# Kernel optimization log

Measured on AMD Instinct MI355X. Metric: run time of the kernel, lower is better.

## Reference

```python
import jax, jax.numpy as jnp
import numpy as np

IN_C = 256
KEY_C = 256
VAL_C = 256
HEADS = 8


def setup_inputs() -> dict:
    key = jax.random.key(0)
    ks = jax.random.split(key, 9)
    s = 0.02
    return {
        "x": jax.random.normal(ks[0], (4, 8192, IN_C), dtype=jnp.float32),
        "Wk": jax.random.normal(ks[1], (KEY_C, IN_C), dtype=jnp.float32) * s,
        "bk": jax.random.normal(ks[2], (KEY_C,), dtype=jnp.float32) * s,
        "Wq": jax.random.normal(ks[3], (KEY_C, IN_C), dtype=jnp.float32) * s,
        "bq": jax.random.normal(ks[4], (KEY_C,), dtype=jnp.float32) * s,
        "Wv": jax.random.normal(ks[5], (VAL_C, IN_C), dtype=jnp.float32) * s,
        "bv": jax.random.normal(ks[6], (VAL_C,), dtype=jnp.float32) * s,
        "Wr": jax.random.normal(ks[7], (IN_C, VAL_C), dtype=jnp.float32) * s,
        "br": jax.random.normal(ks[8], (IN_C,), dtype=jnp.float32) * s,
    }


def reference(x, Wk, bk, Wq, bq, Wv, bv, Wr, br):
    n, N, c = x.shape
    # Faithful to torch: reshape (NOT transpose) of (n, N, c) into (n, c, N)
    xi = x.reshape(n, c, N)
    # 1x1 convs == channel-mixing matmuls over the token axis
    K = jnp.einsum('oc,ncs->nos', Wk, xi) + bk[None, :, None]
    Q = jnp.einsum('oc,ncs->nos', Wq, xi) + bq[None, :, None]
    V = jnp.einsum('oc,ncs->nos', Wv, xi) + bv[None, :, None]
    dk = KEY_C // HEADS
    dv = VAL_C // HEADS
    Kh = K.reshape(n, HEADS, dk, N)
    Qh = Q.reshape(n, HEADS, dk, N)
    Vh = V.reshape(n, HEADS, dv, N)
    # keys: softmax over tokens (dim=2); queries: softmax over head key channels (dim=1)
    Kh = jax.nn.softmax(Kh, axis=3)
    Qh = jax.nn.softmax(Qh, axis=2)
    # context = K @ V^T : [n, H, dk, dv]
    ctx = jnp.einsum('nhks,nhvs->nhkv', Kh, Vh)
    # attended = context^T @ Q : [n, H, dv, N]
    att = jnp.einsum('nhkv,nhks->nhvs', ctx, Qh)
    agg = att.reshape(n, VAL_C, N)
    rep = jnp.einsum('ov,nvs->nos', Wr, agg) + br[None, :, None]
    out = rep + xi  # residual in (n, c, N) layout
    return jnp.transpose(out, (0, 2, 1))  # (n, N, c)
```

## Files before the change

### kernel.cpp

```cpp
#include <hip/hip_runtime.h>

#define NTOK 8192
#define NCH  256
#define TT   64
#define XTP  264
#define EKP  72

typedef unsigned short u16;
typedef __attribute__((ext_vector_type(8))) short bf16x8;
typedef __attribute__((ext_vector_type(4))) float f32x4;
typedef __attribute__((ext_vector_type(8))) unsigned short u16x8;
typedef __attribute__((ext_vector_type(4))) unsigned short u16x4;

__device__ __forceinline__ float b2f(u16 h){
  union{unsigned u; float f;} x; x.u = ((unsigned)h) << 16; return x.f;
}
__device__ __forceinline__ u16 f2b(float f){
  union{float f; unsigned u;} x; x.f = f;
  unsigned u = x.u;
  return (u16)((u + 0x7FFFu + ((u >> 16) & 1u)) >> 16);
}
__device__ __forceinline__ f32x4 mfma16(bf16x8 a, bf16x8 b, f32x4 c){
  return __builtin_amdgcn_mfma_f32_16x16x32_bf16(a, b, c, 0, 0, 0);
}

__device__ __forceinline__ void stage_xtile(const float* __restrict__ xb,
                                            u16* scratch, u16* dst, int t)
{
  #pragma unroll
  for (int i = 0; i < 4; ++i) {
    int ch = i * 64 + (t >> 3);
    int tk = (t & 7) * 8;
    const float* p = xb + (size_t)ch * NTOK + tk;
    float4 v0 = *(const float4*)p;
    float4 v1 = *(const float4*)(p + 4);
    u16x8 pk;
    pk[0]=f2b(v0.x); pk[1]=f2b(v0.y); pk[2]=f2b(v0.z); pk[3]=f2b(v0.w);
    pk[4]=f2b(v1.x); pk[5]=f2b(v1.y); pk[6]=f2b(v1.z); pk[7]=f2b(v1.w);
    *(u16x8*)&scratch[ch * EKP + tk] = pk;
  }
  __syncthreads();
  #pragma unroll
  for (int p = 0; p < 4; ++p) {
    int idx = p * 512 + t;
    int tok = idx & 63;
    int ch = (idx >> 6) * 8;
    u16x8 o;
    #pragma unroll
    for (int j = 0; j < 8; ++j) o[j] = scratch[(ch + j) * EKP + tok];
    *(u16x8*)&dst[tok * XTP + ch] = o;
  }
}

__global__ __launch_bounds__(256)
void k_prep(const float* __restrict__ Wk, const float* __restrict__ Wq,
            const float* __restrict__ Wv, const float* __restrict__ Wr,
            u16* __restrict__ wbf, float* __restrict__ ctxAcc)
{
  const int t = threadIdx.x, bid = blockIdx.x;
  if (bid < 64) {
    const int mat = bid >> 4;
    const float* src = (mat == 0) ? Wk : (mat == 1) ? Wq : (mat == 2) ? Wv : Wr;
    u16* dst = wbf + mat * 65536;
    const int base = (bid & 15) * 4096 + t * 16;
    #pragma unroll
    for (int i = 0; i < 4; ++i) {
      float4 v = *(const float4*)(src + base + i * 4);
      u16x4 pk; pk[0]=f2b(v.x); pk[1]=f2b(v.y); pk[2]=f2b(v.z); pk[3]=f2b(v.w);
      *(u16x4*)(dst + base + i * 4) = pk;
    }
  } else {
    int j = (bid - 64) * 1024 + t * 4;
    float4 z; z.x = z.y = z.z = z.w = 0.f;
    *(float4*)(ctxAcc + j) = z;
  }
}

__global__ __launch_bounds__(512, 4)
void k_ctx(const float* __restrict__ x, const u16* __restrict__ wbf,
           const float* __restrict__ bk, const float* __restrict__ bv,
           float* __restrict__ ctxAcc, float* __restrict__ denomAcc)
{
  __shared__ u16 bufA[NCH * EKP];
  __shared__ u16 ekb[NCH * EKP];

  const int t = threadIdx.x;
  const int b = blockIdx.x >> 7, g = blockIdx.x & 127;
  const int w = t >> 6, lane = t & 63;
  const int l15 = lane & 15, quad = lane >> 4;
  const u16* Wkb = wbf;
  const u16* Wvb = wbf + 2 * 65536;

  stage_xtile(x + (size_t)b * NCH * NTOK + g * TT, ekb, bufA, t);
  __syncthreads();

  f32x4 acc[2][4];

  #pragma unroll
  for (int mi = 0; mi < 2; ++mi)
    #pragma unroll
    for (int nj = 0; nj < 4; ++nj) acc[mi][nj] = (f32x4)0.f;
  for (int k0 = 0; k0 < NCH; k0 += 32) {
    bf16x8 af[2], bx[4];
    #pragma unroll
    for (int mi = 0; mi < 2; ++mi)
      af[mi] = *(const bf16x8*)(Wkb + (size_t)(w * 32 + mi * 16 + l15) * NCH + k0 + quad * 8);
    #pragma unroll
    for (int nj = 0; nj < 4; ++nj)
      bx[nj] = *(const bf16x8*)&bufA[(nj * 16 + l15) * XTP + k0 + quad * 8];
    #pragma unroll
    for (int mi = 0; mi < 2; ++mi)
      #pragma unroll
      for (int nj = 0; nj < 4; ++nj) acc[mi][nj] = mfma16(af[mi], bx[nj], acc[mi][nj]);
  }
  #pragma unroll
  for (int mi = 0; mi < 2; ++mi) {
    float4 bb = *(const float4*)(bk + w * 32 + mi * 16 + quad * 4);
    #pragma unroll
    for (int nj = 0; nj < 4; ++nj) {
      int tok = nj * 16 + l15, chb = w * 32 + mi * 16 + quad * 4;
      ekb[(chb + 0) * EKP + tok] = f2b(__expf(acc[mi][nj][0] + bb.x));
      ekb[(chb + 1) * EKP + tok] = f2b(__expf(acc[mi][nj][1] + bb.y));
      ekb[(chb + 2) * EKP + tok] = f2b(__expf(acc[mi][nj][2] + bb.z));
      ekb[(chb + 3) * EKP + tok] = f2b(__expf(acc[mi][nj][3] + bb.w));
    }
  }

  #pragma unroll
  for (int mi = 0; mi < 2; ++mi)
    #pragma unroll
    for (int nj = 0; nj < 4; ++nj) acc[mi][nj] = (f32x4)0.f;
  for (int k0 = 0; k0 < NCH; k0 += 32) {
    bf16x8 af[2], bx[4];
    #pragma unroll
    for (int mi = 0; mi < 2; ++mi)
      af[mi] = *(const bf16x8*)(Wvb + (size_t)(w * 32 + mi * 16 + l15) * NCH + k0 + quad * 8);
    #pragma unroll
    for (int nj = 0; nj < 4; ++nj)
      bx[nj] = *(const bf16x8*)&bufA[(nj * 16 + l15) * XTP + k0 + quad * 8];
    #pragma unroll
    for (int mi = 0; mi < 2; ++mi)
      #pragma unroll
      for (int nj = 0; nj < 4; ++nj) acc[mi][nj] = mfma16(af[mi], bx[nj], acc[mi][nj]);
  }
  __syncthreads();
  #pragma unroll
  for (int mi = 0; mi < 2; ++mi) {
    float4 bb = *(const float4*)(bv + w * 32 + mi * 16 + quad * 4);
    #pragma unroll
    for (int nj = 0; nj < 4; ++nj) {
      int tok = nj * 16 + l15, chb = w * 32 + mi * 16 + quad * 4;
      bufA[(chb + 0) * EKP + tok] = f2b(acc[mi][nj][0] + bb.x);
      bufA[(chb + 1) * EKP + tok] = f2b(acc[mi][nj][1] + bb.y);
      bufA[(chb + 2) * EKP + tok] = f2b(acc[mi][nj][2] + bb.z);
      bufA[(chb + 3) * EKP + tok] = f2b(acc[mi][nj][3] + bb.w);
    }
  }
  __syncthreads();

  f32x4 cacc[2][2];
  #pragma unroll
  for (int mi = 0; mi < 2; ++mi)
    #pragma unroll
    for (int nj = 0; nj < 2; ++nj) cacc[mi][nj] = (f32x4)0.f;
  #pragma unroll
  for (int kc = 0; kc < 2; ++kc) {
    bf16x8 ae[2], bvv[2];
    #pragma unroll
    for (int mi = 0; mi < 2; ++mi)
      ae[mi] = *(const bf16x8*)&ekb[(w * 32 + mi * 16 + l15) * EKP + kc * 32 + quad * 8];
    #pragma unroll
    for (int nj = 0; nj < 2; ++nj)
      bvv[nj] = *(const bf16x8*)&bufA[(w * 32 + nj * 16 + l15) * EKP + kc * 32 + quad * 8];
    #pragma unroll
    for (int mi = 0; mi < 2; ++mi)
      #pragma unroll
      for (int nj = 0; nj < 2; ++nj)
        cacc[mi][nj] = mfma16(ae[mi], bvv[nj], cacc[mi][nj]);
  }
  float dsum = 0.f;
  if (t < 256) {
    #pragma unroll
    for (int s = 0; s < TT; s += 8) {
      u16x8 v = *(const u16x8*)&ekb[t * EKP + s];
      #pragma unroll
      for (int j = 0; j < 8; ++j) dsum += b2f(v[j]);
    }
  }

  float* cp = ctxAcc + ((size_t)b << 13);
  #pragma unroll
  for (int mi = 0; mi < 2; ++mi)
    #pragma unroll
    for (int nj = 0; nj < 2; ++nj)
      #pragma unroll
      for (int r = 0; r < 4; ++r) {
        int e = ((w * 32 + mi * 16 + quad * 4 + r) << 5) + nj * 16 + l15;
        atomicAdd(&cp[e], cacc[mi][nj][r]);
      }
  if (t < 256)
    atomicAdd(&denomAcc[b * 256 + t], dsum);
}

__global__ __launch_bounds__(512, 4)
void k_out(const float* __restrict__ x, const u16* __restrict__ wbf,
           const float* __restrict__ bq, const float* __restrict__ br,
           const float* __restrict__ ctxAcc, const float* __restrict__ denomAcc,
           float* __restrict__ out)
{
  __shared__ u16 xs[TT * XTP];
  __shared__ u16 qs[NCH * EKP];

  const int t = threadIdx.x;
  const int b = blockIdx.x >> 7, g = blockIdx.x & 127;
  const int w = t >> 6, lane = t & 63;
  const int l15 = lane & 15, quad = lane >> 4;
  const u16* Wqb = wbf + 65536;
  const u16* Wrb = wbf + 3 * 65536;

  stage_xtile(x + (size_t)b * NCH * NTOK + g * TT, qs, xs, t);
  __syncthreads();

  const float* cb = ctxAcc + ((size_t)b << 13) + ((size_t)w << 10);
  bf16x8 ac[2];
  #pragma unroll
  for (int mi = 0; mi < 2; ++mi)
    #pragma unroll
    for (int j = 0; j < 8; ++j)
      ac[mi][j] = (short)f2b(cb[(quad * 8 + j) * 32 + mi * 16 + l15]);

  f32x4 acc[2][4];
  #pragma unroll
  for (int mi = 0; mi < 2; ++mi)
    #pragma unroll
    for (int nj = 0; nj < 4; ++nj) acc[mi][nj] = (f32x4)0.f;
  for (int k0 = 0; k0 < NCH; k0 += 32) {
    bf16x8 af[2], bx[4];
    #pragma unroll
    for (int mi = 0; mi < 2; ++mi)
      af[mi] = *(const bf16x8*)(Wqb + (size_t)(w * 32 + mi * 16 + l15) * NCH + k0 + quad * 8);
    #pragma unroll
    for (int nj = 0; nj < 4; ++nj)
      bx[nj] = *(const bf16x8*)&xs[(nj * 16 + l15) * XTP + k0 + quad * 8];
    #pragma unroll
    for (int mi = 0; mi < 2; ++mi)
      #pragma unroll
      for (int nj = 0; nj < 4; ++nj) acc[mi][nj] = mfma16(af[mi], bx[nj], acc[mi][nj]);
  }
  #pragma unroll
  for (int mi = 0; mi < 2; ++mi) {
    float4 bb = *(const float4*)(bq + w * 32 + mi * 16 + quad * 4);
    #pragma unroll
    for (int nj = 0; nj < 4; ++nj) {
      acc[mi][nj][0] = __expf(acc[mi][nj][0] + bb.x);
      acc[mi][nj][1] = __expf(acc[mi][nj][1] + bb.y);
      acc[mi][nj][2] = __expf(acc[mi][nj][2] + bb.z);
      acc[mi][nj][3] = __expf(acc[mi][nj][3] + bb.w);
    }
  }
  float inv[4];
  #pragma unroll
  for (int nj = 0; nj < 4; ++nj) {
    float s = 0.f;
    #pragma unroll
    for (int mi = 0; mi < 2; ++mi)
      #pragma unroll
      for (int r = 0; r < 4; ++r) s += acc[mi][nj][r];
    s += __shfl_xor(s, 16);
    s += __shfl_xor(s, 32);
    inv[nj] = 1.0f / s;
  }
  #pragma unroll
  for (int mi = 0; mi < 2; ++mi) {
    float4 dv = *(const float4*)(denomAcc + b * 256 + w * 32 + mi * 16 + quad * 4);
    float rdx = 1.0f / dv.x, rdy = 1.0f / dv.y, rdz = 1.0f / dv.z, rdw = 1.0f / dv.w;
    #pragma unroll
    for (int nj = 0; nj < 4; ++nj) {
      u16x4 pk;
      pk[0] = f2b(acc[mi][nj][0] * inv[nj] * rdx);
      pk[1] = f2b(acc[mi][nj][1] * inv[nj] * rdy);
      pk[2] = f2b(acc[mi][nj][2] * inv[nj] * rdz);
      pk[3] = f2b(acc[mi][nj][3] * inv[nj] * rdw);
      *(u16x4*)&qs[(nj * 16 + l15) * XTP + w * 32 + mi * 16 + quad * 4] = pk;
    }
  }
  __syncthreads();

  f32x4 aacc[2][4];
  {
    #pragma unroll
    for (int nj = 0; nj < 4; ++nj) {
      bf16x8 bqf = *(const bf16x8*)&qs[(nj * 16 + l15) * XTP + w * 32 + quad * 8];
      #pragma unroll
      for (int mi = 0; mi < 2; ++mi)
        aacc[mi][nj] = mfma16(ac[mi], bqf, (f32x4)0.f);
    }
  }
  #pragma unroll
  for (int mi = 0; mi < 2; ++mi)
    #pragma unroll
    for (int nj = 0; nj < 4; ++nj) {
      u16x4 pk;
      pk[0] = f2b(aacc[mi][nj][0]);
      pk[1] = f2b(aacc[mi][nj][1]);
      pk[2] = f2b(aacc[mi][nj][2]);
      pk[3] = f2b(aacc[mi][nj][3]);
      *(u16x4*)&qs[(nj * 16 + l15) * XTP + w * 32 + mi * 16 + quad * 4] = pk;
    }
  __syncthreads();

  #pragma unroll
  for (int mi = 0; mi < 2; ++mi)
    #pragma unroll
    for (int nj = 0; nj < 4; ++nj) acc[mi][nj] = (f32x4)0.f;
  for (int k0 = 0; k0 < NCH; k0 += 32) {
    bf16x8 af[2], bx[4];
    #pragma unroll
    for (int mi = 0; mi < 2; ++mi)
      af[mi] = *(const bf16x8*)(Wrb + (size_t)(w * 32 + mi * 16 + l15) * NCH + k0 + quad * 8);
    #pragma unroll
    for (int nj = 0; nj < 4; ++nj)
      bx[nj] = *(const bf16x8*)&qs[(nj * 16 + l15) * XTP + k0 + quad * 8];
    #pragma unroll
    for (int mi = 0; mi < 2; ++mi)
      #pragma unroll
      for (int nj = 0; nj < 4; ++nj) acc[mi][nj] = mfma16(af[mi], bx[nj], acc[mi][nj]);
  }
  #pragma unroll
  for (int mi = 0; mi < 2; ++mi) {
    float4 bb = *(const float4*)(br + w * 32 + mi * 16 + quad * 4);
    #pragma unroll
    for (int nj = 0; nj < 4; ++nj) {
      int tok = nj * 16 + l15;
      u16x4 rx = *(const u16x4*)&xs[tok * XTP + w * 32 + mi * 16 + quad * 4];
      float4 o;
      o.x = acc[mi][nj][0] + bb.x + b2f(rx[0]);
      o.y = acc[mi][nj][1] + bb.y + b2f(rx[1]);
      o.z = acc[mi][nj][2] + bb.z + b2f(rx[2]);
      o.w = acc[mi][nj][3] + bb.w + b2f(rx[3]);
      *(float4*)(out + (((size_t)(b * NTOK + g * TT + tok)) << 8) + w * 32 + mi * 16 + quad * 4) = o;
    }
  }
}

extern "C" void kernel_launch(void* const* d_in, const int* in_sizes, int n_in,
                              void* d_out, int out_size, void* d_ws, size_t ws_size,
                              hipStream_t stream) {
  const float* x  = (const float*)d_in[0];
  const float* Wk = (const float*)d_in[1];
  const float* bk = (const float*)d_in[2];
  const float* Wq = (const float*)d_in[3];
  const float* bq = (const float*)d_in[4];
  const float* Wv = (const float*)d_in[5];
  const float* bv = (const float*)d_in[6];
  const float* Wr = (const float*)d_in[7];
  const float* br = (const float*)d_in[8];
  float* out = (float*)d_out;

  char* wsb = (char*)d_ws;
  float* ctxAcc   = (float*)wsb;
  float* denomAcc = (float*)(wsb + 131072);
  u16*   wbf      = (u16*)(wsb + 135168);

  hipLaunchKernelGGL(k_prep, dim3(97), dim3(256), 0, stream,
                     Wk, Wq, Wv, Wr, wbf, ctxAcc);
  hipLaunchKernelGGL(k_ctx, dim3(512), dim3(512), 0, stream,
                     x, wbf, bk, bv, ctxAcc, denomAcc);
  hipLaunchKernelGGL(k_out, dim3(512), dim3(512), 0, stream,
                     x, wbf, bq, br, ctxAcc, denomAcc, out);
}
```

Measured before the change: 150.9 us.

## Replace global atomics with per-block partials and a separate reduction kernel

k_ctx now writes each block's context partial (as bf16) and its denominator partial to workspace instead of issuing float atomicAdds into a shared accumulator. A new k_red kernel sums the 128 partials per batch, stores the context transposed in bf16 so k_out can load it with one vector load, and precomputes reciprocal denominators. This removes atomic contention and the zero-init pass, at the cost of an extra launch, about 8 MB of partial traffic, and bf16 rounding of the partials before summation.

Result: faster. 144.9 us (-4.0%).

```diff
diff --git a/kernel.cpp b/kernel.cpp
--- a/kernel.cpp
+++ b/kernel.cpp
@@ -55,31 +55,25 @@
 __global__ __launch_bounds__(256)
 void k_prep(const float* __restrict__ Wk, const float* __restrict__ Wq,
             const float* __restrict__ Wv, const float* __restrict__ Wr,
-            u16* __restrict__ wbf, float* __restrict__ ctxAcc)
+            u16* __restrict__ wbf)
 {
   const int t = threadIdx.x, bid = blockIdx.x;
-  if (bid < 64) {
-    const int mat = bid >> 4;
-    const float* src = (mat == 0) ? Wk : (mat == 1) ? Wq : (mat == 2) ? Wv : Wr;
-    u16* dst = wbf + mat * 65536;
-    const int base = (bid & 15) * 4096 + t * 16;
-    #pragma unroll
-    for (int i = 0; i < 4; ++i) {
-      float4 v = *(const float4*)(src + base + i * 4);
-      u16x4 pk; pk[0]=f2b(v.x); pk[1]=f2b(v.y); pk[2]=f2b(v.z); pk[3]=f2b(v.w);
-      *(u16x4*)(dst + base + i * 4) = pk;
-    }
-  } else {
-    int j = (bid - 64) * 1024 + t * 4;
-    float4 z; z.x = z.y = z.z = z.w = 0.f;
-    *(float4*)(ctxAcc + j) = z;
+  const int mat = bid >> 4;
+  const float* src = (mat == 0) ? Wk : (mat == 1) ? Wq : (mat == 2) ? Wv : Wr;
+  u16* dst = wbf + mat * 65536;
+  const int base = (bid & 15) * 4096 + t * 16;
+  #pragma unroll
+  for (int i = 0; i < 4; ++i) {
+    float4 v = *(const float4*)(src + base + i * 4);
+    u16x4 pk; pk[0]=f2b(v.x); pk[1]=f2b(v.y); pk[2]=f2b(v.z); pk[3]=f2b(v.w);
+    *(u16x4*)(dst + base + i * 4) = pk;
   }
 }
 
 __global__ __launch_bounds__(512, 4)
 void k_ctx(const float* __restrict__ x, const u16* __restrict__ wbf,
            const float* __restrict__ bk, const float* __restrict__ bv,
-           float* __restrict__ ctxAcc, float* __restrict__ denomAcc)
+           u16* __restrict__ ctxPart, float* __restrict__ denomPart)
 {
   __shared__ u16 bufA[NCH * EKP];
   __shared__ u16 ekb[NCH * EKP];
@@ -188,7 +182,7 @@
     }
   }
 
-  float* cp = ctxAcc + ((size_t)b << 13);
+  u16* cp = ctxPart + ((size_t)(b * 128 + g) << 13);
   #pragma unroll
   for (int mi = 0; mi < 2; ++mi)
     #pragma unroll
@@ -196,16 +190,45 @@
       #pragma unroll
       for (int r = 0; r < 4; ++r) {
         int e = ((w * 32 + mi * 16 + quad * 4 + r) << 5) + nj * 16 + l15;
-        atomicAdd(&cp[e], cacc[mi][nj][r]);
+        cp[e] = f2b(cacc[mi][nj][r]);
       }
   if (t < 256)
-    atomicAdd(&denomAcc[b * 256 + t], dsum);
+    denomPart[(size_t)(b * 128 + g) * 256 + t] = dsum;
+}
+
+__global__ __launch_bounds__(256)
+void k_red(const u16* __restrict__ ctxPart, const float* __restrict__ denomPart,
+           u16* __restrict__ ctxT, float* __restrict__ rdenomF)
+{
+  int i = blockIdx.x * 256 + threadIdx.x;
+  if (i < 32768) {
+    int b = i >> 13, e = i & 8191;
+    const u16* p = ctxPart + ((size_t)(b * 128) << 13) + e;
+    float s0 = 0.f, s1 = 0.f, s2 = 0.f, s3 = 0.f;
+    #pragma unroll 8
+    for (int g = 0; g < 128; g += 4) {
+      s0 += b2f(p[(size_t)(g + 0) << 13]);
+      s1 += b2f(p[(size_t)(g + 1) << 13]);
+      s2 += b2f(p[(size_t)(g + 2) << 13]);
+      s3 += b2f(p[(size_t)(g + 3) << 13]);
+    }
+    float s = (s0 + s1) + (s2 + s3);
+    int hh = e >> 10, kk = (e >> 5) & 31, vch = e & 31;
+    ctxT[(((b * 8 + hh) * 32 + vch) << 5) + kk] = f2b(s);
+  } else if (i < 33792) {
+    int j = i - 32768, b = j >> 8, ch = j & 255;
+    const float* p = denomPart + (size_t)(b * 128) * 256 + ch;
+    float s = 0.f;
+    #pragma unroll 8
+    for (int g = 0; g < 128; ++g) s += p[(size_t)g << 8];
+    rdenomF[j] = 1.0f / s;
+  }
 }
 
 __global__ __launch_bounds__(512, 4)
 void k_out(const float* __restrict__ x, const u16* __restrict__ wbf,
            const float* __restrict__ bq, const float* __restrict__ br,
-           const float* __restrict__ ctxAcc, const float* __restrict__ denomAcc,
+           const u16* __restrict__ ctxT, const float* __restrict__ rdenomF,
            float* __restrict__ out)
 {
   __shared__ u16 xs[TT * XTP];
@@ -221,13 +244,10 @@
   stage_xtile(x + (size_t)b * NCH * NTOK + g * TT, qs, xs, t);
   __syncthreads();
 
-  const float* cb = ctxAcc + ((size_t)b << 13) + ((size_t)w << 10);
   bf16x8 ac[2];
   #pragma unroll
   for (int mi = 0; mi < 2; ++mi)
-    #pragma unroll
-    for (int j = 0; j < 8; ++j)
-      ac[mi][j] = (short)f2b(cb[(quad * 8 + j) * 32 + mi * 16 + l15]);
+    ac[mi] = *(const bf16x8*)(ctxT + (((size_t)(b * 8 + w) * 32 + mi * 16 + l15) << 5) + quad * 8);
 
   f32x4 acc[2][4];
   #pragma unroll
@@ -272,15 +292,14 @@
   }
   #pragma unroll
   for (int mi = 0; mi < 2; ++mi) {
-    float4 dv = *(const float4*)(denomAcc + b * 256 + w * 32 + mi * 16 + quad * 4);
-    float rdx = 1.0f / dv.x, rdy = 1.0f / dv.y, rdz = 1.0f / dv.z, rdw = 1.0f / dv.w;
+    float4 rd = *(const float4*)(rdenomF + b * 256 + w * 32 + mi * 16 + quad * 4);
     #pragma unroll
     for (int nj = 0; nj < 4; ++nj) {
       u16x4 pk;
-      pk[0] = f2b(acc[mi][nj][0] * inv[nj] * rdx);
-      pk[1] = f2b(acc[mi][nj][1] * inv[nj] * rdy);
-      pk[2] = f2b(acc[mi][nj][2] * inv[nj] * rdz);
-      pk[3] = f2b(acc[mi][nj][3] * inv[nj] * rdw);
+      pk[0] = f2b(acc[mi][nj][0] * inv[nj] * rd.x);
+      pk[1] = f2b(acc[mi][nj][1] * inv[nj] * rd.y);
+      pk[2] = f2b(acc[mi][nj][2] * inv[nj] * rd.z);
+      pk[3] = f2b(acc[mi][nj][3] * inv[nj] * rd.w);
       *(u16x4*)&qs[(nj * 16 + l15) * XTP + w * 32 + mi * 16 + quad * 4] = pk;
     }
   }
@@ -358,14 +377,18 @@
   float* out = (float*)d_out;
 
   char* wsb = (char*)d_ws;
-  float* ctxAcc   = (float*)wsb;
-  float* denomAcc = (float*)(wsb + 131072);
-  u16*   wbf      = (u16*)(wsb + 135168);
-
-  hipLaunchKernelGGL(k_prep, dim3(97), dim3(256), 0, stream,
-                     Wk, Wq, Wv, Wr, wbf, ctxAcc);
+  u16*   ctxPart   = (u16*)wsb;
+  float* denomPart = (float*)(wsb + 8388608);
+  u16*   ctxT      = (u16*)(wsb + 8912896);
+  float* rdenomF   = (float*)(wsb + 8978432);
+  u16*   wbf       = (u16*)(wsb + 8982528);
+
+  hipLaunchKernelGGL(k_prep, dim3(64), dim3(256), 0, stream,
+                     Wk, Wq, Wv, Wr, wbf);
   hipLaunchKernelGGL(k_ctx, dim3(512), dim3(512), 0, stream,
-                     x, wbf, bk, bv, ctxAcc, denomAcc);
+                     x, wbf, bk, bv, ctxPart, denomPart);
+  hipLaunchKernelGGL(k_red, dim3(132), dim3(256), 0, stream,
+                     ctxPart, denomPart, ctxT, rdenomF);
   hipLaunchKernelGGL(k_out, dim3(512), dim3(512), 0, stream,
-                     x, wbf, bq, br, ctxAcc, denomAcc, out);
-}
+                     x, wbf, bq, br, ctxT, rdenomF, out);
+}
```
